# Kernel optimization log

Hardware: AMD Instinct MI355X
Metric: run time of the kernel (lower is better)

Reference implementation:

```python
import jax, jax.numpy as jnp
import numpy as np


def setup_inputs() -> dict:
    key = jax.random.key(0)
    k1, k2 = jax.random.split(key)
    B, T, D, C = 16, 2048, 256, 8
    x = jax.random.normal(k1, (B, T, D), dtype=jnp.float32)
    centers = jax.random.normal(k2, (C, D), dtype=jnp.float32)
    scale = jnp.ones((C,), dtype=jnp.float32)
    return {"x": x, "centers": centers, "scale": scale}


def reference(x, centers, scale):
    # x: (B,T,D), centers: (C,D), scale: (C,)
    # Squared distances ||x - c||^2 via expansion (avoids (B,T,C,D) residual tensor):
    x_sq = jnp.sum(x * x, axis=-1, keepdims=True)          # (B,T,1)
    c_sq = jnp.sum(centers * centers, axis=-1)             # (C,)
    xc = jnp.einsum('btd,cd->btc', x, centers)             # (B,T,C)
    distances = x_sq - 2.0 * xc + c_sq                     # (B,T,C)
    assignment = jax.nn.softmax(-scale * distances, axis=2)  # (B,T,C)
    # sum_t a[b,t,c] * (x[b,t,d] - centers[c,d])
    agg_x = jnp.einsum('btc,btd->bcd', assignment, x)      # (B,C,D)
    a_sum = jnp.sum(assignment, axis=1)                    # (B,C)
    aggregated = agg_x - a_sum[..., None] * centers        # (B,C,D)
    B = x.shape[0]
    return aggregated.reshape(B, -1)
```

## Files before the change

kernel.cpp:

```cpp
#include <hip/hip_runtime.h>
#include <stdint.h>
#include <stddef.h>

#define DD   256
#define CC   8
#define RPB  32
#define RPW  8
#define XROW 264
#define NBLK 1024

#define GLOAD16(g, l) __builtin_amdgcn_global_load_lds(                      \
    (const __attribute__((address_space(1))) void*)(g),                      \
    (__attribute__((address_space(3))) void*)(l), 16, 0, 0)

__device__ __forceinline__ float dot4(float4 a, float4 b) {
  return a.x * b.x + a.y * b.y + a.z * b.z + a.w * b.w;
}

__global__ __launch_bounds__(256) void lde_main(
    const float* __restrict__ x,
    const float* __restrict__ centers,
    const float* __restrict__ scale,
    float* __restrict__ pa,
    float* __restrict__ pas)
{
  __shared__ __align__(16) float x_lds[RPB * XROW];
  __shared__ __align__(16) float c_lds[CC * DD];
  __shared__ __align__(16) float a_lds[RPB * CC];

  const int tid  = threadIdx.x;
  const int lane = tid & 63;
  const int wave = tid >> 6;
  const int blk  = blockIdx.x;

  float sv[CC];
  #pragma unroll
  for (int c = 0; c < CC; ++c) sv[c] = scale[c];

  {
    const int  lrow0 = wave * RPW;
    const long grow0 = (long)blk * RPB + lrow0;
    #pragma unroll
    for (int r = 0; r < RPW; ++r) {
      const float* g = x + (grow0 + r) * DD + lane * 4;
      GLOAD16(g, &x_lds[(lrow0 + r) * XROW]);
    }
  }

  {
    const float4* cg = (const float4*)centers;
    float4* cl = (float4*)c_lds;
    cl[tid]       = cg[tid];
    cl[tid + 256] = cg[tid + 256];
  }

  asm volatile("s_waitcnt vmcnt(0)" ::: "memory");
  __syncthreads();

  float cs = 0.f;
  {
    const int c = lane >> 3, oo = lane & 7;
    #pragma unroll
    for (int k = 0; k < 8; ++k) {
      float4 cv = *(const float4*)&c_lds[c * DD + k * 32 + oo * 4];
      cs += dot4(cv, cv);
    }
    cs += __shfl_xor(cs, 1);
    cs += __shfl_xor(cs, 2);
    cs += __shfl_xor(cs, 4);
  }
  float csqv[CC];
  #pragma unroll
  for (int c = 0; c < CC; ++c) csqv[c] = __shfl(cs, c * 8);

  const int o    = lane & 7;
  const int rl   = lane >> 3;
  const int lrow = wave * RPW + rl;
  {
    const float* xr = &x_lds[lrow * XROW];
    float dots[CC] = {0.f, 0.f, 0.f, 0.f, 0.f, 0.f, 0.f, 0.f};
    float xsq = 0.f;
    #pragma unroll
    for (int k = 0; k < 8; ++k) {
      float4 xv = *(const float4*)&xr[k * 32 + o * 4];
      xsq += dot4(xv, xv);
      #pragma unroll
      for (int c = 0; c < CC; ++c) {
        float4 cv = *(const float4*)&c_lds[c * DD + k * 32 + o * 4];
        dots[c] += dot4(xv, cv);
      }
    }
    xsq += __shfl_xor(xsq, 1);
    xsq += __shfl_xor(xsq, 2);
    xsq += __shfl_xor(xsq, 4);
    #pragma unroll
    for (int c = 0; c < CC; ++c) {
      dots[c] += __shfl_xor(dots[c], 1);
      dots[c] += __shfl_xor(dots[c], 2);
      dots[c] += __shfl_xor(dots[c], 4);
    }

    float lgt[CC], m = -1e30f;
    #pragma unroll
    for (int c = 0; c < CC; ++c) {
      lgt[c] = -sv[c] * (xsq - 2.f * dots[c] + csqv[c]);
      m = fmaxf(m, lgt[c]);
    }
    float e[CC], ssum = 0.f;
    #pragma unroll
    for (int c = 0; c < CC; ++c) { e[c] = __expf(lgt[c] - m); ssum += e[c]; }
    const float inv = 1.f / ssum;
    float eo = (o == 0) ? e[0] : (o == 1) ? e[1] : (o == 2) ? e[2] : (o == 3) ? e[3]
             : (o == 4) ? e[4] : (o == 5) ? e[5] : (o == 6) ? e[6] : e[7];
    a_lds[lrow * CC + o] = eo * inv;
  }
  __syncthreads();

  if (wave == 0) {
    const int c = lane >> 3, oo = lane & 7;
    float s = 0.f;
    #pragma unroll
    for (int j = 0; j < 4; ++j) s += a_lds[(j * 8 + oo) * CC + c];
    s += __shfl_xor(s, 1);
    s += __shfl_xor(s, 2);
    s += __shfl_xor(s, 4);
    if (oo == 0) pas[blk * CC + c] = s;
  }

  {
    const int d = wave * 64 + lane;
    float acc[CC] = {0.f, 0.f, 0.f, 0.f, 0.f, 0.f, 0.f, 0.f};
    #pragma unroll
    for (int r = 0; r < RPB; ++r) {
      const float  xv = x_lds[r * XROW + d];
      const float4 a0 = *(const float4*)&a_lds[r * CC];
      const float4 a1 = *(const float4*)&a_lds[r * CC + 4];
      acc[0] += a0.x * xv; acc[1] += a0.y * xv; acc[2] += a0.z * xv; acc[3] += a0.w * xv;
      acc[4] += a1.x * xv; acc[5] += a1.y * xv; acc[6] += a1.z * xv; acc[7] += a1.w * xv;
    }
    float* pab = pa + (size_t)blk * (CC * DD);
    #pragma unroll
    for (int c = 0; c < CC; ++c) pab[c * DD + d] = acc[c];
  }
}

__global__ __launch_bounds__(256) void lde_finalize(
    const float* __restrict__ pa,
    const float* __restrict__ pas,
    const float* __restrict__ centers,
    float* __restrict__ out)
{
  const int b    = blockIdx.x >> 3;
  const int c    = blockIdx.x & 7;
  const int d    = threadIdx.x;
  const int lane = threadIdx.x & 63;

  float v = pas[(b * 64 + lane) * CC + c];
  v += __shfl_xor(v, 1);
  v += __shfl_xor(v, 2);
  v += __shfl_xor(v, 4);
  v += __shfl_xor(v, 8);
  v += __shfl_xor(v, 16);
  v += __shfl_xor(v, 32);

  float s = 0.f;
  #pragma unroll 8
  for (int k = 0; k < 64; ++k)
    s += pa[((size_t)(b * 64 + k) * CC + c) * DD + d];

  out[(b * CC + c) * DD + d] = s - v * centers[c * DD + d];
}

extern "C" void kernel_launch(void* const* d_in, const int* in_sizes, int n_in,
                              void* d_out, int out_size, void* d_ws, size_t ws_size,
                              hipStream_t stream)
{
  const float* x       = (const float*)d_in[0];
  const float* centers = (const float*)d_in[1];
  const float* scale   = (const float*)d_in[2];
  float* out = (float*)d_out;

  float* pa  = (float*)d_ws;
  float* pas = pa + (size_t)NBLK * CC * DD;

  lde_main<<<NBLK, 256, 0, stream>>>(x, centers, scale, pa, pas);
  lde_finalize<<<128, 256, 0, stream>>>(pa, pas, centers, out);
}
```

Before: 88.77 us.

## Double rows per block, restructure aggregation with per-wave tiles and LDS reduction

Each block now handles 64 rows, so the grid halves to 512 blocks and each wave computes distances for two rows per lane group, reusing every center load twice. The weighted aggregation changes shape: each wave accumulates float4 columns over its own 16 rows, taking the assignment weights by shuffle, then the four waves reduce through LDS. This halves the partial-sum traffic to the workspace. The partials are stored c-major so the finalize kernel can do vectorized float4 reductions split across waves. The cost is more LDS per block (about 76KB), which limits residency to fewer blocks per CU, plus more registers per thread.

```diff
diff --git a/kernel.cpp b/kernel.cpp
--- a/kernel.cpp
+++ b/kernel.cpp
@@ -4,10 +4,11 @@
 
 #define DD   256
 #define CC   8
-#define RPB  32
-#define RPW  8
+#define BB   16
+#define RPB  64
+#define NBLK 512
+#define KPB  32
 #define XROW 264
-#define NBLK 1024
 
 #define GLOAD16(g, l) __builtin_amdgcn_global_load_lds(                      \
     (const __attribute__((address_space(1))) void*)(g),                      \
@@ -38,28 +39,27 @@
   for (int c = 0; c < CC; ++c) sv[c] = scale[c];
 
   {
-    const int  lrow0 = wave * RPW;
+    const int  lrow0 = wave * 16;
     const long grow0 = (long)blk * RPB + lrow0;
     #pragma unroll
-    for (int r = 0; r < RPW; ++r) {
+    for (int r = 0; r < 16; ++r) {
       const float* g = x + (grow0 + r) * DD + lane * 4;
       GLOAD16(g, &x_lds[(lrow0 + r) * XROW]);
     }
   }
-
   {
     const float4* cg = (const float4*)centers;
     float4* cl = (float4*)c_lds;
     cl[tid]       = cg[tid];
     cl[tid + 256] = cg[tid + 256];
   }
-
   asm volatile("s_waitcnt vmcnt(0)" ::: "memory");
   __syncthreads();
 
-  float cs = 0.f;
+  float csqv[CC];
   {
     const int c = lane >> 3, oo = lane & 7;
+    float cs = 0.f;
     #pragma unroll
     for (int k = 0; k < 8; ++k) {
       float4 cv = *(const float4*)&c_lds[c * DD + k * 32 + oo * 4];
@@ -68,51 +68,65 @@
     cs += __shfl_xor(cs, 1);
     cs += __shfl_xor(cs, 2);
     cs += __shfl_xor(cs, 4);
-  }
-  float csqv[CC];
-  #pragma unroll
-  for (int c = 0; c < CC; ++c) csqv[c] = __shfl(cs, c * 8);
-
-  const int o    = lane & 7;
-  const int rl   = lane >> 3;
-  const int lrow = wave * RPW + rl;
-  {
-    const float* xr = &x_lds[lrow * XROW];
-    float dots[CC] = {0.f, 0.f, 0.f, 0.f, 0.f, 0.f, 0.f, 0.f};
-    float xsq = 0.f;
+    #pragma unroll
+    for (int cc = 0; cc < CC; ++cc) csqv[cc] = __shfl(cs, cc * 8);
+  }
+
+  {
+    const int o  = lane & 7;
+    const int rl = lane >> 3;
+    const int r0 = wave * 16 + rl;
+    const float* xr0 = &x_lds[r0 * XROW];
+    const float* xr1 = &x_lds[(r0 + 8) * XROW];
+
+    float d0[CC] = {0,0,0,0,0,0,0,0};
+    float d1[CC] = {0,0,0,0,0,0,0,0};
+    float xq0 = 0.f, xq1 = 0.f;
     #pragma unroll
     for (int k = 0; k < 8; ++k) {
-      float4 xv = *(const float4*)&xr[k * 32 + o * 4];
-      xsq += dot4(xv, xv);
+      const float4 xv0 = *(const float4*)&xr0[k * 32 + o * 4];
+      const float4 xv1 = *(const float4*)&xr1[k * 32 + o * 4];
+      xq0 += dot4(xv0, xv0);
+      xq1 += dot4(xv1, xv1);
       #pragma unroll
       for (int c = 0; c < CC; ++c) {
-        float4 cv = *(const float4*)&c_lds[c * DD + k * 32 + o * 4];
-        dots[c] += dot4(xv, cv);
+        const float4 cv = *(const float4*)&c_lds[c * DD + k * 32 + o * 4];
+        d0[c] += dot4(xv0, cv);
+        d1[c] += dot4(xv1, cv);
       }
     }
-    xsq += __shfl_xor(xsq, 1);
-    xsq += __shfl_xor(xsq, 2);
-    xsq += __shfl_xor(xsq, 4);
+    xq0 += __shfl_xor(xq0, 1); xq0 += __shfl_xor(xq0, 2); xq0 += __shfl_xor(xq0, 4);
+    xq1 += __shfl_xor(xq1, 1); xq1 += __shfl_xor(xq1, 2); xq1 += __shfl_xor(xq1, 4);
     #pragma unroll
     for (int c = 0; c < CC; ++c) {
-      dots[c] += __shfl_xor(dots[c], 1);
-      dots[c] += __shfl_xor(dots[c], 2);
-      dots[c] += __shfl_xor(dots[c], 4);
-    }
-
-    float lgt[CC], m = -1e30f;
-    #pragma unroll
-    for (int c = 0; c < CC; ++c) {
-      lgt[c] = -sv[c] * (xsq - 2.f * dots[c] + csqv[c]);
-      m = fmaxf(m, lgt[c]);
-    }
-    float e[CC], ssum = 0.f;
-    #pragma unroll
-    for (int c = 0; c < CC; ++c) { e[c] = __expf(lgt[c] - m); ssum += e[c]; }
-    const float inv = 1.f / ssum;
-    float eo = (o == 0) ? e[0] : (o == 1) ? e[1] : (o == 2) ? e[2] : (o == 3) ? e[3]
-             : (o == 4) ? e[4] : (o == 5) ? e[5] : (o == 6) ? e[6] : e[7];
-    a_lds[lrow * CC + o] = eo * inv;
+      d0[c] += __shfl_xor(d0[c], 1); d0[c] += __shfl_xor(d0[c], 2); d0[c] += __shfl_xor(d0[c], 4);
+      d1[c] += __shfl_xor(d1[c], 1); d1[c] += __shfl_xor(d1[c], 2); d1[c] += __shfl_xor(d1[c], 4);
+    }
+
+    {
+      float lgt[CC], m = -1e30f;
+      #pragma unroll
+      for (int c = 0; c < CC; ++c) { lgt[c] = -sv[c] * (xq0 - 2.f * d0[c] + csqv[c]); m = fmaxf(m, lgt[c]); }
+      float e[CC], ssum = 0.f;
+      #pragma unroll
+      for (int c = 0; c < CC; ++c) { e[c] = __expf(lgt[c] - m); ssum += e[c]; }
+      const float inv = 1.f / ssum;
+      float eo = (o == 0) ? e[0] : (o == 1) ? e[1] : (o == 2) ? e[2] : (o == 3) ? e[3]
+               : (o == 4) ? e[4] : (o == 5) ? e[5] : (o == 6) ? e[6] : e[7];
+      a_lds[r0 * CC + o] = eo * inv;
+    }
+    {
+      float lgt[CC], m = -1e30f;
+      #pragma unroll
+      for (int c = 0; c < CC; ++c) { lgt[c] = -sv[c] * (xq1 - 2.f * d1[c] + csqv[c]); m = fmaxf(m, lgt[c]); }
+      float e[CC], ssum = 0.f;
+      #pragma unroll
+      for (int c = 0; c < CC; ++c) { e[c] = __expf(lgt[c] - m); ssum += e[c]; }
+      const float inv = 1.f / ssum;
+      float eo = (o == 0) ? e[0] : (o == 1) ? e[1] : (o == 2) ? e[2] : (o == 3) ? e[3]
+               : (o == 4) ? e[4] : (o == 5) ? e[5] : (o == 6) ? e[6] : e[7];
+      a_lds[(r0 + 8) * CC + o] = eo * inv;
+    }
   }
   __syncthreads();
 
@@ -120,27 +134,49 @@
     const int c = lane >> 3, oo = lane & 7;
     float s = 0.f;
     #pragma unroll
-    for (int j = 0; j < 4; ++j) s += a_lds[(j * 8 + oo) * CC + c];
+    for (int j = 0; j < 8; ++j) s += a_lds[(j * 8 + oo) * CC + c];
     s += __shfl_xor(s, 1);
     s += __shfl_xor(s, 2);
     s += __shfl_xor(s, 4);
-    if (oo == 0) pas[blk * CC + c] = s;
-  }
-
-  {
-    const int d = wave * 64 + lane;
-    float acc[CC] = {0.f, 0.f, 0.f, 0.f, 0.f, 0.f, 0.f, 0.f};
-    #pragma unroll
-    for (int r = 0; r < RPB; ++r) {
-      const float  xv = x_lds[r * XROW + d];
-      const float4 a0 = *(const float4*)&a_lds[r * CC];
-      const float4 a1 = *(const float4*)&a_lds[r * CC + 4];
-      acc[0] += a0.x * xv; acc[1] += a0.y * xv; acc[2] += a0.z * xv; acc[3] += a0.w * xv;
-      acc[4] += a1.x * xv; acc[5] += a1.y * xv; acc[6] += a1.z * xv; acc[7] += a1.w * xv;
-    }
-    float* pab = pa + (size_t)blk * (CC * DD);
-    #pragma unroll
-    for (int c = 0; c < CC; ++c) pab[c * DD + d] = acc[c];
+    if (oo == 0) pas[c * NBLK + blk] = s;
+  }
+
+  float4 acc[CC];
+  #pragma unroll
+  for (int c = 0; c < CC; ++c) acc[c] = make_float4(0.f, 0.f, 0.f, 0.f);
+  {
+    const float2 av = *(const float2*)&a_lds[(wave * 16 + (lane >> 2)) * CC + (lane & 3) * 2];
+    #pragma unroll
+    for (int r = 0; r < 16; ++r) {
+      const float4 xv = *(const float4*)&x_lds[(wave * 16 + r) * XROW + lane * 4];
+      #pragma unroll
+      for (int c = 0; c < CC; ++c) {
+        const float a = __shfl((c & 1) ? av.y : av.x, r * 4 + (c >> 1));
+        acc[c].x += a * xv.x; acc[c].y += a * xv.y; acc[c].z += a * xv.z; acc[c].w += a * xv.w;
+      }
+    }
+  }
+  __syncthreads();
+
+  float* p_lds = x_lds;
+  #pragma unroll
+  for (int c = 0; c < CC; ++c)
+    *(float4*)&p_lds[(wave * CC + c) * DD + lane * 4] = acc[c];
+  __syncthreads();
+  {
+    const int c = tid >> 5;
+    const int g = tid & 31;
+    #pragma unroll
+    for (int h = 0; h < 2; ++h) {
+      const int d4 = g + 32 * h;
+      float4 s0 = *(const float4*)&p_lds[(0 * CC + c) * DD + d4 * 4];
+      float4 s1 = *(const float4*)&p_lds[(1 * CC + c) * DD + d4 * 4];
+      float4 s2 = *(const float4*)&p_lds[(2 * CC + c) * DD + d4 * 4];
+      float4 s3 = *(const float4*)&p_lds[(3 * CC + c) * DD + d4 * 4];
+      float4 s = make_float4(s0.x + s1.x + s2.x + s3.x, s0.y + s1.y + s2.y + s3.y,
+                             s0.z + s1.z + s2.z + s3.z, s0.w + s1.w + s2.w + s3.w);
+      *(float4*)&pa[((size_t)c * NBLK + blk) * DD + d4 * 4] = s;
+    }
   }
 }
 
@@ -150,25 +186,36 @@
     const float* __restrict__ centers,
     float* __restrict__ out)
 {
-  const int b    = blockIdx.x >> 3;
-  const int c    = blockIdx.x & 7;
-  const int d    = threadIdx.x;
-  const int lane = threadIdx.x & 63;
-
-  float v = pas[(b * 64 + lane) * CC + c];
-  v += __shfl_xor(v, 1);
-  v += __shfl_xor(v, 2);
-  v += __shfl_xor(v, 4);
-  v += __shfl_xor(v, 8);
-  v += __shfl_xor(v, 16);
-  v += __shfl_xor(v, 32);
-
-  float s = 0.f;
-  #pragma unroll 8
-  for (int k = 0; k < 64; ++k)
-    s += pa[((size_t)(b * 64 + k) * CC + c) * DD + d];
-
-  out[(b * CC + c) * DD + d] = s - v * centers[c * DD + d];
+  __shared__ __align__(16) float r_lds[4][DD];
+  const int b  = blockIdx.x >> 3;
+  const int c  = blockIdx.x & 7;
+  const int kq = threadIdx.x >> 6;
+  const int d4 = threadIdx.x & 63;
+
+  const float* base = pa + ((size_t)c * NBLK + b * KPB) * DD;
+  float4 s = make_float4(0.f, 0.f, 0.f, 0.f);
+  #pragma unroll
+  for (int j = 0; j < 8; ++j) {
+    const float4 v = *(const float4*)&base[(kq * 8 + j) * DD + d4 * 4];
+    s.x += v.x; s.y += v.y; s.z += v.z; s.w += v.w;
+  }
+  *(float4*)&r_lds[kq][d4 * 4] = s;
+  __syncthreads();
+
+  if (kq == 0) {
+    float4 t0 = *(const float4*)&r_lds[0][d4 * 4];
+    float4 t1 = *(const float4*)&r_lds[1][d4 * 4];
+    float4 t2 = *(const float4*)&r_lds[2][d4 * 4];
+    float4 t3 = *(const float4*)&r_lds[3][d4 * 4];
+    float4 t = make_float4(t0.x + t1.x + t2.x + t3.x, t0.y + t1.y + t2.y + t3.y,
+                           t0.z + t1.z + t2.z + t3.z, t0.w + t1.w + t2.w + t3.w);
+    float v = pas[c * NBLK + b * KPB + (d4 & 31)];
+    v += __shfl_xor(v, 1); v += __shfl_xor(v, 2); v += __shfl_xor(v, 4);
+    v += __shfl_xor(v, 8); v += __shfl_xor(v, 16);
+    const float4 cv = *(const float4*)&centers[c * DD + d4 * 4];
+    float4 o4 = make_float4(t.x - v * cv.x, t.y - v * cv.y, t.z - v * cv.z, t.w - v * cv.w);
+    *(float4*)&out[(size_t)(b * CC + c) * DD + d4 * 4] = o4;
+  }
 }
 
 extern "C" void kernel_launch(void* const* d_in, const int* in_sizes, int n_in,
@@ -181,8 +228,8 @@
   float* out = (float*)d_out;
 
   float* pa  = (float*)d_ws;
-  float* pas = pa + (size_t)NBLK * CC * DD;
+  float* pas = pa + (size_t)CC * NBLK * DD;
 
   lde_main<<<NBLK, 256, 0, stream>>>(x, centers, scale, pa, pas);
-  lde_finalize<<<128, 256, 0, stream>>>(pa, pas, centers, out);
-}
+  lde_finalize<<<BB * CC, 256, 0, stream>>>(pa, pas, centers, out);
+}
```

New measurement: 85.98 us. -3.1%, faster.
